# Performance work log

Hardware: AMD Instinct MI355X
Metric: run time of the kernel (lower is better)

The kernel has to match this reference:

```python
import jax, jax.numpy as jnp
import numpy as np

B, N, C, H = 16, 577, 768, 12  # batch, tokens (384px ViT-B/16 + cls), dim, heads


def setup_inputs() -> dict:
    key = jax.random.key(0)
    k0, k1, k2, k3, k4 = jax.random.split(key, 5)
    x = jax.random.normal(k0, (B, N, C), dtype=jnp.float32)
    Wqkv = jax.random.normal(k1, (3 * C, C), dtype=jnp.float32) * 0.02   # nn.Linear(dim, 3*dim, bias=False)
    Wproj = jax.random.normal(k2, (C, C), dtype=jnp.float32) * 0.02      # nn.Linear(dim, dim)
    bproj = jnp.zeros((C,), dtype=jnp.float32)
    Wpre = jax.random.normal(k3, (H, H), dtype=jnp.float32) * (1.0 / np.sqrt(H))   # proj_pre, bias=False
    Wpost = jax.random.normal(k4, (H, H), dtype=jnp.float32) * (1.0 / np.sqrt(H))  # proj_post, bias=False
    return {"x": x, "Wqkv": Wqkv, "Wproj": Wproj, "bproj": bproj, "Wpre": Wpre, "Wpost": Wpost}


def reference(x, Wqkv, Wproj, bproj, Wpre, Wpost):
    b, n, c = x.shape
    h = Wpre.shape[0]
    d = c // h
    scale = d ** -0.5
    # qkv projection: [B,N,3,H,d]
    qkv = (x @ Wqkv.T).reshape(b, n, 3, h, d)
    q = qkv[:, :, 0]  # [B,N,H,d]
    k = qkv[:, :, 1]
    v = qkv[:, :, 2]
    # scaled dot-product logits: [B,H,N,N]
    attn = jnp.einsum('bnhd,bmhd->bhnm', q, k) * scale
    # pre-softmax talking-heads mixing: Linear over head axis, y_g = sum_h x_h * Wpre[g,h]
    attn = jnp.einsum('bhnm,gh->bgnm', attn, Wpre)
    attn = jax.nn.softmax(attn, axis=-1)
    # post-softmax talking-heads mixing
    attn = jnp.einsum('bhnm,gh->bgnm', attn, Wpost)
    # weighted values -> [B,N,C]
    out = jnp.einsum('bhnm,bmhd->bnhd', attn, v).reshape(b, n, c)
    # output projection (dropout is identity at inference / p given but attn_drop forced 0.0)
    return out @ Wproj.T + bproj
```

## Files before the change

### kernel.cpp

```cpp
#include <hip/hip_runtime.h>
#include <hip/hip_bf16.h>

#define NTOK 577
#define CH 768
#define NH 12
#define HD 64
#define M_ROWS 9232
#define NPAD 592
#define ESP 72
#define EST 18944

#define XHE 7090176
#define WQH 1769472
#define WPH 589824

typedef _Float16 f16x8 __attribute__((ext_vector_type(8)));
typedef _Float16 f16x4 __attribute__((ext_vector_type(4)));
typedef _Float16 f16x2 __attribute__((ext_vector_type(2)));
typedef float f32x4 __attribute__((ext_vector_type(4)));

#define MFMA16(a, b, c) __builtin_amdgcn_mfma_f32_16x16x32_f16((a), (b), (c), 0, 0, 0)

#define BAR() asm volatile("s_waitcnt lgkmcnt(0)\n\ts_barrier" ::: "memory")

#define GLD16(gp, lp) __builtin_amdgcn_global_load_lds(               \
    (const __attribute__((address_space(1))) void*)(gp),              \
    (__attribute__((address_space(3))) void*)(lp), 16, 0, 0)

__device__ __forceinline__ int xcd_swz(int lin, int G) {
  int q = G >> 3, r = G & 7;
  int x = lin & 7, i = lin >> 3;
  return (x < r ? x * (q + 1) : r * (q + 1) + (x - r) * q) + i;
}

__device__ __forceinline__ float bf2f(unsigned int u16) {
  union { unsigned int i; float f; } x; x.i = u16 << 16; return x.f;
}

__device__ __forceinline__ float ldin(const void* p, size_t i, bool f32) {
  return f32 ? ((const float*)p)[i]
             : __bfloat162float(((const __hip_bfloat16*)p)[i]);
}

__device__ __forceinline__ f16x8 ld8_cvt(const void* p, size_t idx, bool f32) {
  f16x8 r;
  if (f32) {
    const float* f = (const float*)p + idx;
    const float4 u = *(const float4*)f;
    const float4 v = *(const float4*)(f + 4);
    r[0]=(_Float16)u.x; r[1]=(_Float16)u.y; r[2]=(_Float16)u.z; r[3]=(_Float16)u.w;
    r[4]=(_Float16)v.x; r[5]=(_Float16)v.y; r[6]=(_Float16)v.z; r[7]=(_Float16)v.w;
  } else {
    const unsigned short* s = (const unsigned short*)p + idx;
    uint4 u = *(const uint4*)s;
    unsigned int w0=u.x, w1=u.y, w2=u.z, w3=u.w;
    r[0]=(_Float16)bf2f(w0&0xffffu); r[1]=(_Float16)bf2f(w0>>16);
    r[2]=(_Float16)bf2f(w1&0xffffu); r[3]=(_Float16)bf2f(w1>>16);
    r[4]=(_Float16)bf2f(w2&0xffffu); r[5]=(_Float16)bf2f(w2>>16);
    r[6]=(_Float16)bf2f(w3&0xffffu); r[7]=(_Float16)bf2f(w3>>16);
  }
  return r;
}

__global__ void detect_dtype(const unsigned short* __restrict__ xs,
                             int* __restrict__ flag) {
  __shared__ int cnt;
  if (threadIdx.x == 0) cnt = 0;
  __syncthreads();
  int local = 0;
  for (int i = threadIdx.x; i < 4096; i += 256) {
    unsigned int u = xs[2 * i];
    unsigned int e = (u >> 7) & 0xFFu;
    if (e >= 140u) local++;
  }
  atomicAdd(&cnt, local);
  __syncthreads();
  if (threadIdx.x == 0) *flag = (cnt > 100) ? 1 : 0;
}

__global__ __launch_bounds__(256) void cvt_all(
    const void* __restrict__ x, const void* __restrict__ wq,
    const void* __restrict__ wp, _Float16* __restrict__ dst,
    const int* __restrict__ flagp)
{
  const bool f32 = (*flagp != 0);
  size_t i = (size_t)(blockIdx.x * 256 + threadIdx.x) * 8;
  if (i >= (size_t)(XHE + WQH + WPH)) return;
  const void* src; size_t off;
  if (i < XHE)            { src = x;  off = i; }
  else if (i < XHE + WQH) { src = wq; off = i - XHE; }
  else                    { src = wp; off = i - XHE - WQH; }
  *(f16x8*)(dst + i) = ld8_cvt(src, off, f32);
}

__global__ __launch_bounds__(256) void gemm_qkv_mfma(
    const _Float16* __restrict__ X, const _Float16* __restrict__ W,
    _Float16* __restrict__ q, _Float16* __restrict__ k,
    _Float16* __restrict__ vT)
{
  __shared__ __align__(16) _Float16 As[2][128 * 32];
  __shared__ __align__(16) _Float16 Bs[2][128 * 32];
  const int swz = xcd_swz(blockIdx.x, 18 * 73);
  const int bx = swz % 18;
  const int m0 = (swz / 18) * 128;
  const int tid = threadIdx.x;
  const int lane = tid & 63, wave = tid >> 6;
  const int quad = lane >> 4, l16 = lane & 15;
  const int wm = wave & 1, wo = wave >> 1;
  const int t = bx / 6;
  const int o0 = bx * 128;
  const int o0loc = o0 - t * CH;

  const int row0 = wave * 32 + (lane >> 2);
  const int ch8  = (((lane & 3) ^ ((lane >> 3) & 3)) << 3);
  const int ar0 = min(m0 + row0, M_ROWS - 1);
  const int ar1 = min(m0 + row0 + 16, M_ROWS - 1);
  const int br0 = o0 + row0;
  const int br1 = o0 + row0 + 16;
  const int dl0 = wave * 1024 + lane * 8;
  const int dl1 = dl0 + 512;

  GLD16(X + (size_t)ar0 * CH + ch8, &As[0][dl0]);
  GLD16(X + (size_t)ar1 * CH + ch8, &As[0][dl1]);
  GLD16(W + (size_t)br0 * CH + ch8, &Bs[0][dl0]);
  GLD16(W + (size_t)br1 * CH + ch8, &Bs[0][dl1]);

  const int rdc = ((quad ^ ((l16 >> 1) & 3)) << 3);
  const int rdA = (wm * 64 + l16) * 32 + rdc;
  const int rdB = (wo * 64 + l16) * 32 + rdc;

  f32x4 acc[4][4] = {};
  int cur = 0;
  for (int ks = 0; ks < CH / 32; ++ks) {
    __syncthreads();
    if (ks + 1 < CH / 32) {
      const int kc = (ks + 1) * 32 + ch8;
      const int nb = cur ^ 1;
      GLD16(X + (size_t)ar0 * CH + kc, &As[nb][dl0]);
      GLD16(X + (size_t)ar1 * CH + kc, &As[nb][dl1]);
      GLD16(W + (size_t)br0 * CH + kc, &Bs[nb][dl0]);
      GLD16(W + (size_t)br1 * CH + kc, &Bs[nb][dl1]);
    }
    f16x8 af[4], bf_[4];
    #pragma unroll
    for (int i = 0; i < 4; ++i)
      af[i] = *(const f16x8*)&As[cur][rdA + i * 512];
    #pragma unroll
    for (int j = 0; j < 4; ++j)
      bf_[j] = *(const f16x8*)&Bs[cur][rdB + j * 512];
    #pragma unroll
    for (int i = 0; i < 4; ++i)
      #pragma unroll
      for (int j = 0; j < 4; ++j)
        acc[i][j] = MFMA16(af[i], bf_[j], acc[i][j]);
    cur ^= 1;
  }

  if (t < 2) {
    _Float16* dbuf = (t == 0) ? q : k;
    const int ntl = (t == 0) ? 37 : 40;
    #pragma unroll
    for (int i = 0; i < 4; ++i) {
      #pragma unroll
      for (int rr = 0; rr < 4; ++rr) {
        int m = m0 + wm * 64 + i * 16 + quad * 4 + rr;
        if (m >= M_ROWS) continue;
        int b = m / NTOK, n = m - b * NTOK;
        #pragma unroll
        for (int j = 0; j < 4; ++j) {
          int o = o0loc + wo * 64 + j * 16 + l16;
          int h = o >> 6, dd = o & 63;
          dbuf[((size_t)(b * NH + h) * ntl + (n >> 4)) * 1024
               + (dd >> 3) * 128 + (n & 15) * 8 + (dd & 7)] =
              (_Float16)acc[i][j][rr];
        }
      }
    }
  } else {
    __syncthreads();
    _Float16* scrb = &As[0][0] + wave * 512;
    #pragma unroll
    for (int i = 0; i < 4; ++i) {
      #pragma unroll
      for (int j = 0; j < 4; ++j) {
        _Float16* scr = scrb + (j & 1) * 256;
        f16x4 wv;
        wv[0] = (_Float16)acc[i][j][0]; wv[1] = (_Float16)acc[i][j][1];
        wv[2] = (_Float16)acc[i][j][2]; wv[3] = (_Float16)acc[i][j][3];
        *(f16x4*)&scr[l16 * 16 + quad * 4] = wv;
        asm volatile("s_waitcnt lgkmcnt(0)" ::: "memory");
        f16x4 rv = *(const f16x4*)&scr[(lane >> 2) * 16 + (lane & 3) * 4];
        int oc = o0loc + wo * 64 + j * 16 + (lane >> 2);
        int hh = oc >> 6, ddg = oc & 63;
        int mbase = m0 + wm * 64 + i * 16 + (lane & 3) * 4;
        int bb = mbase / NTOK, nn2 = mbase - bb * NTOK;
        if (mbase + 3 < M_ROWS && nn2 + 3 < NTOK && !(nn2 & 1)
            && (nn2 & 31) <= 28) {
          _Float16* dst = &vT[((size_t)(bb * NH + hh) * 20 + (nn2 >> 5)) * 2048
                              + ddg * 32 + (nn2 & 31)];
          f16x2 lo2, hi2;
          lo2[0] = rv[0]; lo2[1] = rv[1];
          hi2[0] = rv[2]; hi2[1] = rv[3];
          *(f16x2*)dst = lo2;
          *(f16x2*)(dst + 2) = hi2;
        } else {
          #pragma unroll
          for (int e = 0; e < 4; ++e) {
            int m = mbase + e;
            if (m < M_ROWS) {
              int b2 = m / NTOK, n2 = m - b2 * NTOK;
              vT[((size_t)(b2 * NH + hh) * 20 + (n2 >> 5)) * 2048
                 + ddg * 32 + (n2 & 31)] = rv[e];
            }
          }
        }
      }
    }
  }
}

__global__ void zerofill_pads(_Float16* __restrict__ vT,
                              _Float16* __restrict__ qF,
                              _Float16* __restrict__ kF) {
  const int NV = 16 * NH * HD * 63;
  const int NK = 16 * NH * 63 * 64;
  const int NQ = 16 * NH * 15 * 64;
  int idx = blockIdx.x * 256 + threadIdx.x;
  if (idx < NV) {
    int r = idx / 63, c = idx % 63;
    int m = NTOK + c;
    int bg = r >> 6, d = r & 63;
    vT[((size_t)bg * 20 + (m >> 5)) * 2048 + d * 32 + (m & 31)] = (_Float16)0.f;
  } else if (idx < NV + NK) {
    int u = idx - NV;
    int bh = u / (63 * 64), v = u % (63 * 64);
    int m = NTOK + v / 64, d = v % 64;
    kF[((size_t)bh * 40 + (m >> 4)) * 1024
       + (d >> 3) * 128 + (m & 15) * 8 + (d & 7)] = (_Float16)0.f;
  } else if (idx < NV + NK + NQ) {
    int u = idx - NV - NK;
    int bh = u / (15 * 64), v = u % (15 * 64);
    int n = NTOK + v / 64, d = v % 64;
    qF[((size_t)bh * 37 + (n >> 4)) * 1024
       + (d >> 3) * 128 + (n & 15) * 8 + (d & 7)] = (_Float16)0.f;
  }
}

__global__ __launch_bounds__(256) void qk_exp(
    const _Float16* __restrict__ q, const _Float16* __restrict__ k,
    const void* __restrict__ Wpre, const int* __restrict__ flagp,
    _Float16* __restrict__ E, float* __restrict__ Rp, int b0, int cb)
{
  const bool f32 = (*flagp != 0);
  __shared__ float wp[NH * NH];
  __shared__ _Float16 Es[NH * 16 * ESP];
  const int tid = threadIdx.x;
  if (tid < NH * NH) wp[tid] = ldin(Wpre, tid, f32) * 0.125f;
  __syncthreads();
  const int swz = xcd_swz(blockIdx.x, 370 * cb);
  const int bl = swz / 370;
  const int ny = (swz % 370) / 10;
  const int bx = swz % 10;
  const int lane = tid & 63, wave = tid >> 6;
  const int quad = lane >> 4, l16 = lane & 15;
  const int b = b0 + bl;
  const int n0 = ny * 16;
  const int m0 = bx * 64 + wave * 16;
  const _Float16* qp0 = q + ((size_t)(b * NH) * 37 + ny) * 1024 + lane * 8;
  const _Float16* kp0 = k + ((size_t)(b * NH) * 40 + bx * 4 + wave) * 1024
                          + lane * 8;
  f32x4 acc[NH];
  #pragma unroll
  for (int h = 0; h < NH; ++h) {
    const _Float16* qp = qp0 + (size_t)h * (37 * 1024);
    const _Float16* kp = kp0 + (size_t)h * (40 * 1024);
    f16x8 a0 = *(const f16x8*)qp;
    f16x8 bb0 = *(const f16x8*)kp;
    f16x8 a1 = *(const f16x8*)(qp + 512);
    f16x8 bb1 = *(const f16x8*)(kp + 512);
    f32x4 z = {0.f, 0.f, 0.f, 0.f};
    z = MFMA16(a0, bb0, z);
    acc[h] = MFMA16(a1, bb1, z);
  }
  const int mloc = wave * 16 + l16;
  const bool valid = (m0 + l16 < NTOK);
  #pragma unroll
  for (int g = 0; g < NH; ++g) {
    float s0 = 0.f, s1 = 0.f, s2 = 0.f, s3 = 0.f;
    #pragma unroll
    for (int h = 0; h < NH; ++h) {
      float w = wp[g * NH + h];
      s0 += w * acc[h][0]; s1 += w * acc[h][1];
      s2 += w * acc[h][2]; s3 += w * acc[h][3];
    }
    Es[(g * 16 + quad * 4 + 0) * ESP + mloc] = (_Float16)(valid ? __expf(s0) : 0.f);
    Es[(g * 16 + quad * 4 + 1) * ESP + mloc] = (_Float16)(valid ? __expf(s1) : 0.f);
    Es[(g * 16 + quad * 4 + 2) * ESP + mloc] = (_Float16)(valid ? __expf(s2) : 0.f);
    Es[(g * 16 + quad * 4 + 3) * ESP + mloc] = (_Float16)(valid ? __expf(s3) : 0.f);
  }
  __syncthreads();
  const int sub2 = tid & 3;
  const int nrow = (tid >> 2) & 15;
  const int rg0  = tid >> 6;
  #pragma unroll
  for (int it = 0; it < 6; ++it) {
    int region = it * 4 + rg0;
    int g = region >> 1, half = region & 1;
    f16x8 vv = *(const f16x8*)&Es[(g * 16 + nrow) * ESP + half * 32 + sub2 * 8];
    *(f16x8*)&E[((size_t)(bl * NH + g) * 20 + bx * 2 + half) * EST
                + (n0 + nrow) * 32 + sub2 * 8] = vv;
  }
  if (tid < NH * 16) {
    const _Float16* row = &Es[tid * ESP];
    float tot = 0.f;
    #pragma unroll
    for (int c = 0; c < 8; ++c) {
      f16x8 t = *(const f16x8*)&row[c * 8];
      #pragma unroll
      for (int j = 0; j < 8; ++j) tot += (float)t[j];
    }
    Rp[(((size_t)b * NH + (tid >> 4)) * 10 + bx) * NPAD + n0 + (tid & 15)] = tot;
  }
}

__global__ __launch_bounds__(256) void pv_mix3(
    const _Float16* __restrict__ E, const _Float16* __restrict__ vT,
    const float* __restrict__ Rp, const void* __restrict__ Wpost,
    const int* __restrict__ flagp, _Float16* __restrict__ o1, int b0, int cb)
{
  const bool f32 = (*flagp != 0);
  __shared__ _Float16 P2s[NH * 8 * 128];
  __shared__ _Float16 w2s[NH * NH];
  __shared__ _Float16 rinvs[NH * 8];
  const int swz = xcd_swz(blockIdx.x, 73 * cb);
  const int bl = swz / 73;
  const int nx = swz % 73;
  const int tid = threadIdx.x;
  const int lane = tid & 63, w = tid >> 6;
  const int quad = lane >> 4, l16 = lane & 15;
  const int nn = l16 & 7;
  const int n0 = nx * 8;
  const int b = b0 + bl;
  if (tid < NH * NH) w2s[tid] = (_Float16)ldin(Wpost, tid, f32);
  if (tid < NH * 8) {
    float tot = 0.f;
    #pragma unroll
    for (int mb = 0; mb < 10; ++mb)
      tot += Rp[(((size_t)b * NH + (tid >> 3)) * 10 + mb) * NPAD + n0 + (tid & 7)];
    rinvs[tid] = (_Float16)(tot > 0.f ? 1.f / tot : 0.f);
  }
  __syncthreads();
  _Float16 rloc[NH];
  #pragma unroll
  for (int h = 0; h < NH; ++h) rloc[h] = rinvs[h * 8 + nn];

  f32x4 O[3][4];
  #pragma unroll
  for (int j = 0; j < 3; ++j)
    #pragma unroll
    for (int dt = 0; dt < 4; ++dt) O[j][dt] = (f32x4){0.f, 0.f, 0.f, 0.f};
  const int gg0 = w * 3;
  const int swzc = nn << 3;

  const size_t eoff = (size_t)(n0 + nn) * 32 + quad * 8;
  const size_t ehead = (size_t)20 * EST;
  const size_t ebl = (size_t)(bl * NH) * ehead;
  f16x8 ev0[NH], ev1[NH];
  #pragma unroll
  for (int h = 0; h < NH; ++h)
    ev0[h] = *(const f16x8*)&E[ebl + h * ehead + (size_t)w * EST + eoff];
  #pragma unroll
  for (int i = 0; i < 5; ++i) {
    f16x8* curp = (i & 1) ? ev1 : ev0;
    f16x8* nxtp = (i & 1) ? ev0 : ev1;
    BAR();
    if (i + 1 < 5) {
      #pragma unroll
      for (int h = 0; h < NH; ++h)
        nxtp[h] = *(const f16x8*)&E[ebl + h * ehead
                                    + (size_t)((i + 1) * 4 + w) * EST + eoff];
    }
    #pragma unroll
    for (int h = 0; h < NH; ++h) curp[h] *= rloc[h];
    #pragma unroll
    for (int gp = 0; gp < NH; ++gp) {
      f16x8 p = curp[0] * w2s[gp * NH + 0];
      #pragma unroll
      for (int h = 1; h < NH; ++h) p += curp[h] * w2s[gp * NH + h];
      if (l16 < 8)
        *(f16x8*)&P2s[gp * 1024 + nn * 128 + ((w * 32 + quad * 8) ^ swzc)] = p;
    }
    BAR();
    #pragma unroll
    for (int kc = 0; kc < 4; ++kc) {
      #pragma unroll
      for (int j = 0; j < 3; ++j) {
        const int g = gg0 + j;
        f16x8 a = *(const f16x8*)&P2s[g * 1024 + nn * 128
                                      + ((kc * 32 + quad * 8) ^ swzc)];
        #pragma unroll
        for (int dt = 0; dt < 4; ++dt) {
          f16x8 bv = *(const f16x8*)(
              vT + ((size_t)(b * NH + g) * 20 + i * 4 + kc) * 2048
                 + (dt * 16 + l16) * 32 + quad * 8);
          O[j][dt] = MFMA16(a, bv, O[j][dt]);
        }
      }
    }
  }
  #pragma unroll
  for (int j = 0; j < 3; ++j)
    #pragma unroll
    for (int dt = 0; dt < 4; ++dt)
      #pragma unroll
      for (int r = 0; r < 4; ++r) {
        int n = quad * 4 + r;
        if (n < 8 && n0 + n < NTOK)
          o1[((size_t)b * NTOK + n0 + n) * CH + (gg0 + j) * HD + dt * 16 + l16] =
              (_Float16)O[j][dt][r];
      }
}

__global__ __launch_bounds__(256) void gemm_proj_mfma(
    const _Float16* __restrict__ A, const _Float16* __restrict__ W,
    const void* __restrict__ bias, const int* __restrict__ flagp,
    void* __restrict__ out)
{
  const bool f32 = (*flagp != 0);
  __shared__ __align__(16) _Float16 As[2][128 * 32];
  __shared__ __align__(16) _Float16 Bs[2][128 * 32];
  const int swz = xcd_swz(blockIdx.x, 6 * 73);
  const int o0 = (swz % 6) * 128;
  const int m0 = (swz / 6) * 128;
  const int tid = threadIdx.x;
  const int lane = tid & 63, wave = tid >> 6;
  const int quad = lane >> 4, l16 = lane & 15;
  const int wm = wave & 1, wo = wave >> 1;

  const int row0 = wave * 32 + (lane >> 2);
  const int ch8  = (((lane & 3) ^ ((lane >> 3) & 3)) << 3);
  const int ar0 = min(m0 + row0, M_ROWS - 1);
  const int ar1 = min(m0 + row0 + 16, M_ROWS - 1);
  const int br0 = o0 + row0;
  const int br1 = o0 + row0 + 16;
  const int dl0 = wave * 1024 + lane * 8;
  const int dl1 = dl0 + 512;

  GLD16(A + (size_t)ar0 * CH + ch8, &As[0][dl0]);
  GLD16(A + (size_t)ar1 * CH + ch8, &As[0][dl1]);
  GLD16(W + (size_t)br0 * CH + ch8, &Bs[0][dl0]);
  GLD16(W + (size_t)br1 * CH + ch8, &Bs[0][dl1]);

  const int rdc = ((quad ^ ((l16 >> 1) & 3)) << 3);
  const int rdA = (wm * 64 + l16) * 32 + rdc;
  const int rdB = (wo * 64 + l16) * 32 + rdc;

  f32x4 acc[4][4] = {};
  int cur = 0;
  for (int ks = 0; ks < CH / 32; ++ks) {
    __syncthreads();
    if (ks + 1 < CH / 32) {
      const int kc = (ks + 1) * 32 + ch8;
      const int nb = cur ^ 1;
      GLD16(A + (size_t)ar0 * CH + kc, &As[nb][dl0]);
      GLD16(A + (size_t)ar1 * CH + kc, &As[nb][dl1]);
      GLD16(W + (size_t)br0 * CH + kc, &Bs[nb][dl0]);
      GLD16(W + (size_t)br1 * CH + kc, &Bs[nb][dl1]);
    }
    f16x8 af[4], bf_[4];
    #pragma unroll
    for (int i = 0; i < 4; ++i)
      af[i] = *(const f16x8*)&As[cur][rdA + i * 512];
    #pragma unroll
    for (int j = 0; j < 4; ++j)
      bf_[j] = *(const f16x8*)&Bs[cur][rdB + j * 512];
    #pragma unroll
    for (int i = 0; i < 4; ++i)
      #pragma unroll
      for (int j = 0; j < 4; ++j)
        acc[i][j] = MFMA16(af[i], bf_[j], acc[i][j]);
    cur ^= 1;
  }

  #pragma unroll
  for (int i = 0; i < 4; ++i) {
    #pragma unroll
    for (int rr = 0; rr < 4; ++rr) {
      int m = m0 + wm * 64 + i * 16 + quad * 4 + rr;
      if (m >= M_ROWS) continue;
      #pragma unroll
      for (int j = 0; j < 4; ++j) {
        int o = o0 + wo * 64 + j * 16 + l16;
        float val = acc[i][j][rr] + ldin(bias, o, f32);
        if (f32) ((float*)out)[(size_t)m * CH + o] = val;
        else ((__hip_bfloat16*)out)[(size_t)m * CH + o] = __float2bfloat16(val);
      }
    }
  }
}

extern "C" void kernel_launch(void* const* d_in, const int* in_sizes, int n_in,
                              void* d_out, int out_size, void* d_ws, size_t ws_size,
                              hipStream_t stream) {
  const void* x     = d_in[0];
  const void* Wqkv  = d_in[1];
  const void* Wproj = d_in[2];
  const void* bproj = d_in[3];
  const void* Wpre  = d_in[4];
  const void* Wpost = d_in[5];

  int* flag = (int*)d_ws;
  _Float16* ws = (_Float16*)((char*)d_ws + 16);
  const size_t QFE = (size_t)16 * NH * 37 * 1024;
  const size_t KFE = (size_t)16 * NH * 40 * 1024;
  const size_t VTE = (size_t)16 * NH * 20 * 2048;
  const size_t OE  = (size_t)M_ROWS * CH;
  const size_t RPE = (size_t)16 * NH * 10 * NPAD;
  const size_t EPB = (size_t)NH * 20 * EST;

  _Float16* Xh  = ws;
  _Float16* Wqh = Xh + XHE;
  _Float16* Wph = Wqh + WQH;
  _Float16* q   = Wph + WPH;
  _Float16* k   = q + QFE;
  _Float16* vT  = k + KFE;
  _Float16* o1  = vT + VTE;
  float*    Rp  = (float*)(o1 + OE);

  const size_t fixedB = 16 + ((size_t)XHE + WQH + WPH + QFE + KFE + VTE + OE)
                             * sizeof(_Float16) + RPE * sizeof(float);
  const size_t perB   = EPB * sizeof(_Float16);
  int cb = 16;
  while (cb > 1 && fixedB + (size_t)cb * perB > ws_size) cb >>= 1;

  _Float16* E = (_Float16*)(Rp + RPE);

  dim3 blk(256);
  hipLaunchKernelGGL(detect_dtype, dim3(1), blk, 0, stream,
                     (const unsigned short*)x, flag);
  hipLaunchKernelGGL(cvt_all, dim3((XHE + WQH + WPH) / 8 / 256 + 1), blk, 0,
                     stream, x, Wqkv, Wproj, Xh, flag);
  hipLaunchKernelGGL(gemm_qkv_mfma, dim3(18 * 73), blk, 0, stream,
                     Xh, Wqh, q, k, vT);
  {
    const int NPADS = 16 * NH * HD * 63 + 16 * NH * 63 * 64 + 16 * NH * 15 * 64;
    hipLaunchKernelGGL(zerofill_pads, dim3((NPADS + 255) / 256), blk, 0,
                       stream, vT, q, k);
  }
  for (int b0 = 0; b0 < 16; b0 += cb) {
    hipLaunchKernelGGL(qk_exp, dim3(370 * cb), blk, 0, stream,
                       q, k, Wpre, flag, E, Rp, b0, cb);
    hipLaunchKernelGGL(pv_mix3, dim3(73 * cb), blk, 0, stream,
                       E, vT, Rp, Wpost, flag, o1, b0, cb);
  }
  hipLaunchKernelGGL(gemm_proj_mfma, dim3(6 * 73), blk, 0, stream,
                     o1, Wph, bproj, flag, d_out);
}
```

Measured before the change: 396.3 us.

## Split PV kernel over key range with 16-row tiles, sum partials in proj GEMM

The PV/post-mix kernel now handles 16 query rows per block instead of 8, so all 16 MFMA rows carry useful data. The key dimension is split into two chunks (3 and 2 of 5 steps), and each chunk writes its own fp16 partial output buffer. The output-projection GEMM loads both partial buffers and adds them while staging A into LDS, replacing the async global-to-LDS copy with register loads. This trades an extra partial buffer, extra global reads and fp16 summation rounding for full MFMA tiles and more parallelism in the PV stage.

New measurement: 381.9 us. 1.04x faster.

```diff
diff --git a/kernel.cpp b/kernel.cpp
--- a/kernel.cpp
+++ b/kernel.cpp
@@ -323,72 +323,37 @@
   }
 }
 
-__global__ __launch_bounds__(256) void pv_mix3(
+template<int NC, int D0>
+__device__ __forceinline__ void pv4_body(
     const _Float16* __restrict__ E, const _Float16* __restrict__ vT,
-    const float* __restrict__ Rp, const void* __restrict__ Wpost,
-    const int* __restrict__ flagp, _Float16* __restrict__ o1, int b0, int cb)
+    _Float16* P2s, const _Float16* w2s, const _Float16* rloc,
+    f32x4 (&O)[3][4], size_t ebl, size_t ehead, size_t eoff,
+    int b, int w, int quad, int l16, int gg0, int swzc)
 {
-  const bool f32 = (*flagp != 0);
-  __shared__ _Float16 P2s[NH * 8 * 128];
-  __shared__ _Float16 w2s[NH * NH];
-  __shared__ _Float16 rinvs[NH * 8];
-  const int swz = xcd_swz(blockIdx.x, 73 * cb);
-  const int bl = swz / 73;
-  const int nx = swz % 73;
-  const int tid = threadIdx.x;
-  const int lane = tid & 63, w = tid >> 6;
-  const int quad = lane >> 4, l16 = lane & 15;
-  const int nn = l16 & 7;
-  const int n0 = nx * 8;
-  const int b = b0 + bl;
-  if (tid < NH * NH) w2s[tid] = (_Float16)ldin(Wpost, tid, f32);
-  if (tid < NH * 8) {
-    float tot = 0.f;
-    #pragma unroll
-    for (int mb = 0; mb < 10; ++mb)
-      tot += Rp[(((size_t)b * NH + (tid >> 3)) * 10 + mb) * NPAD + n0 + (tid & 7)];
-    rinvs[tid] = (_Float16)(tot > 0.f ? 1.f / tot : 0.f);
-  }
-  __syncthreads();
-  _Float16 rloc[NH];
-  #pragma unroll
-  for (int h = 0; h < NH; ++h) rloc[h] = rinvs[h * 8 + nn];
-
-  f32x4 O[3][4];
-  #pragma unroll
-  for (int j = 0; j < 3; ++j)
-    #pragma unroll
-    for (int dt = 0; dt < 4; ++dt) O[j][dt] = (f32x4){0.f, 0.f, 0.f, 0.f};
-  const int gg0 = w * 3;
-  const int swzc = nn << 3;
-
-  const size_t eoff = (size_t)(n0 + nn) * 32 + quad * 8;
-  const size_t ehead = (size_t)20 * EST;
-  const size_t ebl = (size_t)(bl * NH) * ehead;
   f16x8 ev0[NH], ev1[NH];
   #pragma unroll
   for (int h = 0; h < NH; ++h)
-    ev0[h] = *(const f16x8*)&E[ebl + h * ehead + (size_t)w * EST + eoff];
-  #pragma unroll
-  for (int i = 0; i < 5; ++i) {
+    ev0[h] = *(const f16x8*)&E[ebl + h * ehead + (size_t)(D0 * 4 + w) * EST + eoff];
+  #pragma unroll
+  for (int i = 0; i < NC; ++i) {
+    const int dmt = D0 + i;
     f16x8* curp = (i & 1) ? ev1 : ev0;
     f16x8* nxtp = (i & 1) ? ev0 : ev1;
-    BAR();
-    if (i + 1 < 5) {
+    if (i + 1 < NC) {
       #pragma unroll
       for (int h = 0; h < NH; ++h)
         nxtp[h] = *(const f16x8*)&E[ebl + h * ehead
-                                    + (size_t)((i + 1) * 4 + w) * EST + eoff];
+                                    + (size_t)((dmt + 1) * 4 + w) * EST + eoff];
     }
     #pragma unroll
     for (int h = 0; h < NH; ++h) curp[h] *= rloc[h];
+    BAR();
     #pragma unroll
     for (int gp = 0; gp < NH; ++gp) {
       f16x8 p = curp[0] * w2s[gp * NH + 0];
       #pragma unroll
       for (int h = 1; h < NH; ++h) p += curp[h] * w2s[gp * NH + h];
-      if (l16 < 8)
-        *(f16x8*)&P2s[gp * 1024 + nn * 128 + ((w * 32 + quad * 8) ^ swzc)] = p;
+      *(f16x8*)&P2s[gp * 2048 + l16 * 128 + ((w * 32 + quad * 8) ^ swzc)] = p;
     }
     BAR();
     #pragma unroll
@@ -396,35 +361,90 @@
       #pragma unroll
       for (int j = 0; j < 3; ++j) {
         const int g = gg0 + j;
-        f16x8 a = *(const f16x8*)&P2s[g * 1024 + nn * 128
+        f16x8 a = *(const f16x8*)&P2s[g * 2048 + l16 * 128
                                       + ((kc * 32 + quad * 8) ^ swzc)];
         #pragma unroll
         for (int dt = 0; dt < 4; ++dt) {
           f16x8 bv = *(const f16x8*)(
-              vT + ((size_t)(b * NH + g) * 20 + i * 4 + kc) * 2048
+              vT + ((size_t)(b * NH + g) * 20 + dmt * 4 + kc) * 2048
                  + (dt * 16 + l16) * 32 + quad * 8);
           O[j][dt] = MFMA16(a, bv, O[j][dt]);
         }
       }
     }
   }
+}
+
+__global__ __launch_bounds__(256) void pv_mix4(
+    const _Float16* __restrict__ E, const _Float16* __restrict__ vT,
+    const float* __restrict__ Rp, const void* __restrict__ Wpost,
+    const int* __restrict__ flagp, _Float16* __restrict__ Op0,
+    _Float16* __restrict__ Op1, int b0, int cb)
+{
+  const bool f32 = (*flagp != 0);
+  __shared__ _Float16 P2s[NH * 16 * 128];
+  __shared__ _Float16 w2s[NH * NH];
+  __shared__ _Float16 rinvs[NH * 16];
+  const int swz = xcd_swz(blockIdx.x, 74 * cb);
+  const int bl = swz / 74;
+  const int rem = swz % 74;
+  const int z = rem / 37;
+  const int nx = rem % 37;
+  const int tid = threadIdx.x;
+  const int lane = tid & 63, w = tid >> 6;
+  const int quad = lane >> 4, l16 = lane & 15;
+  const int n0 = nx * 16;
+  const int b = b0 + bl;
+  if (tid < NH * NH) w2s[tid] = (_Float16)ldin(Wpost, tid, f32);
+  if (tid < NH * 16) {
+    float tot = 0.f;
+    #pragma unroll
+    for (int mb = 0; mb < 10; ++mb)
+      tot += Rp[(((size_t)b * NH + (tid >> 4)) * 10 + mb) * NPAD + n0 + (tid & 15)];
+    rinvs[tid] = (_Float16)(tot > 0.f ? 1.f / tot : 0.f);
+  }
+  __syncthreads();
+  _Float16 rloc[NH];
+  #pragma unroll
+  for (int h = 0; h < NH; ++h) rloc[h] = rinvs[h * 16 + l16];
+
+  f32x4 O[3][4];
   #pragma unroll
   for (int j = 0; j < 3; ++j)
     #pragma unroll
+    for (int dt = 0; dt < 4; ++dt) O[j][dt] = (f32x4){0.f, 0.f, 0.f, 0.f};
+  const int gg0 = w * 3;
+  const int swzc = (l16 & 7) << 3;
+
+  const size_t eoff = (size_t)(n0 + l16) * 32 + quad * 8;
+  const size_t ehead = (size_t)20 * EST;
+  const size_t ebl = (size_t)(bl * NH) * ehead;
+
+  if (z == 0)
+    pv4_body<3, 0>(E, vT, P2s, w2s, rloc, O, ebl, ehead, eoff,
+                   b, w, quad, l16, gg0, swzc);
+  else
+    pv4_body<2, 3>(E, vT, P2s, w2s, rloc, O, ebl, ehead, eoff,
+                   b, w, quad, l16, gg0, swzc);
+
+  _Float16* __restrict__ Op = z ? Op1 : Op0;
+  #pragma unroll
+  for (int j = 0; j < 3; ++j)
+    #pragma unroll
     for (int dt = 0; dt < 4; ++dt)
       #pragma unroll
       for (int r = 0; r < 4; ++r) {
-        int n = quad * 4 + r;
-        if (n < 8 && n0 + n < NTOK)
-          o1[((size_t)b * NTOK + n0 + n) * CH + (gg0 + j) * HD + dt * 16 + l16] =
+        int nl = quad * 4 + r;
+        if (n0 + nl < NTOK)
+          Op[((size_t)b * NTOK + n0 + nl) * CH + (gg0 + j) * HD + dt * 16 + l16] =
               (_Float16)O[j][dt][r];
       }
 }
 
 __global__ __launch_bounds__(256) void gemm_proj_mfma(
-    const _Float16* __restrict__ A, const _Float16* __restrict__ W,
-    const void* __restrict__ bias, const int* __restrict__ flagp,
-    void* __restrict__ out)
+    const _Float16* __restrict__ A0, const _Float16* __restrict__ A1,
+    const _Float16* __restrict__ W, const void* __restrict__ bias,
+    const int* __restrict__ flagp, void* __restrict__ out)
 {
   const bool f32 = (*flagp != 0);
   __shared__ __align__(16) _Float16 As[2][128 * 32];
@@ -446,8 +466,14 @@
   const int dl0 = wave * 1024 + lane * 8;
   const int dl1 = dl0 + 512;
 
-  GLD16(A + (size_t)ar0 * CH + ch8, &As[0][dl0]);
-  GLD16(A + (size_t)ar1 * CH + ch8, &As[0][dl1]);
+  {
+    f16x8 p00 = *(const f16x8*)(A0 + (size_t)ar0 * CH + ch8);
+    f16x8 p01 = *(const f16x8*)(A1 + (size_t)ar0 * CH + ch8);
+    f16x8 p10 = *(const f16x8*)(A0 + (size_t)ar1 * CH + ch8);
+    f16x8 p11 = *(const f16x8*)(A1 + (size_t)ar1 * CH + ch8);
+    *(f16x8*)&As[0][dl0] = p00 + p01;
+    *(f16x8*)&As[0][dl1] = p10 + p11;
+  }
   GLD16(W + (size_t)br0 * CH + ch8, &Bs[0][dl0]);
   GLD16(W + (size_t)br1 * CH + ch8, &Bs[0][dl1]);
 
@@ -459,13 +485,19 @@
   int cur = 0;
   for (int ks = 0; ks < CH / 32; ++ks) {
     __syncthreads();
-    if (ks + 1 < CH / 32) {
+    f16x8 s0, s1;
+    const bool more = (ks + 1 < CH / 32);
+    if (more) {
       const int kc = (ks + 1) * 32 + ch8;
       const int nb = cur ^ 1;
-      GLD16(A + (size_t)ar0 * CH + kc, &As[nb][dl0]);
-      GLD16(A + (size_t)ar1 * CH + kc, &As[nb][dl1]);
       GLD16(W + (size_t)br0 * CH + kc, &Bs[nb][dl0]);
       GLD16(W + (size_t)br1 * CH + kc, &Bs[nb][dl1]);
+      f16x8 p00 = *(const f16x8*)(A0 + (size_t)ar0 * CH + kc);
+      f16x8 p01 = *(const f16x8*)(A1 + (size_t)ar0 * CH + kc);
+      f16x8 p10 = *(const f16x8*)(A0 + (size_t)ar1 * CH + kc);
+      f16x8 p11 = *(const f16x8*)(A1 + (size_t)ar1 * CH + kc);
+      s0 = p00 + p01;
+      s1 = p10 + p11;
     }
     f16x8 af[4], bf_[4];
     #pragma unroll
@@ -474,6 +506,11 @@
     #pragma unroll
     for (int j = 0; j < 4; ++j)
       bf_[j] = *(const f16x8*)&Bs[cur][rdB + j * 512];
+    if (more) {
+      const int nb = cur ^ 1;
+      *(f16x8*)&As[nb][dl0] = s0;
+      *(f16x8*)&As[nb][dl1] = s1;
+    }
     #pragma unroll
     for (int i = 0; i < 4; ++i)
       #pragma unroll
@@ -524,10 +561,11 @@
   _Float16* q   = Wph + WPH;
   _Float16* k   = q + QFE;
   _Float16* vT  = k + KFE;
-  _Float16* o1  = vT + VTE;
-  float*    Rp  = (float*)(o1 + OE);
-
-  const size_t fixedB = 16 + ((size_t)XHE + WQH + WPH + QFE + KFE + VTE + OE)
+  _Float16* Op0 = vT + VTE;
+  _Float16* Op1 = Op0 + OE;
+  float*    Rp  = (float*)(Op1 + OE);
+
+  const size_t fixedB = 16 + ((size_t)XHE + WQH + WPH + QFE + KFE + VTE + 2 * OE)
                              * sizeof(_Float16) + RPE * sizeof(float);
   const size_t perB   = EPB * sizeof(_Float16);
   int cb = 16;
@@ -550,9 +588,9 @@
   for (int b0 = 0; b0 < 16; b0 += cb) {
     hipLaunchKernelGGL(qk_exp, dim3(370 * cb), blk, 0, stream,
                        q, k, Wpre, flag, E, Rp, b0, cb);
-    hipLaunchKernelGGL(pv_mix3, dim3(73 * cb), blk, 0, stream,
-                       E, vT, Rp, Wpost, flag, o1, b0, cb);
+    hipLaunchKernelGGL(pv_mix4, dim3(74 * cb), blk, 0, stream,
+                       E, vT, Rp, Wpost, flag, Op0, Op1, b0, cb);
   }
   hipLaunchKernelGGL(gemm_proj_mfma, dim3(6 * 73), blk, 0, stream,
-                     o1, Wph, bproj, flag, d_out);
-}
+                     Op0, Op1, Wph, bproj, flag, d_out);
+}
```
